# Performance work log

Hardware: AMD Instinct MI355X
Metric: run time of the kernel (lower is better)

## Reference

```python
import jax, jax.numpy as jnp
import numpy as np

NUM_EXPERTS = 8
HIDDEN = 1024
INTER = 2048
TOKENS = 2048
TOP_K = 2


def setup_inputs() -> dict:
    key = jax.random.key(0)
    k1, k2, k3, k4, k5 = jax.random.split(key, 5)
    hidden_states = jax.random.normal(k1, (TOKENS, HIDDEN), dtype=jnp.float32)
    top_k_index = jax.random.randint(k2, (TOKENS, TOP_K), 0, NUM_EXPERTS, dtype=jnp.int64)
    top_k_weights = jax.random.uniform(k3, (TOKENS, TOP_K), dtype=jnp.float32)
    # parameters, scaled like typical init
    gate_up_proj = jax.random.normal(k4, (NUM_EXPERTS, 2 * INTER, HIDDEN), dtype=jnp.float32) * (HIDDEN ** -0.5)
    down_proj = jax.random.normal(k5, (NUM_EXPERTS, HIDDEN, INTER), dtype=jnp.float32) * (INTER ** -0.5)
    return {
        "hidden_states": hidden_states,
        "top_k_index": top_k_index,
        "top_k_weights": top_k_weights,
        "gate_up_proj": gate_up_proj,
        "down_proj": down_proj,
    }


def reference(hidden_states, top_k_index, top_k_weights, gate_up_proj, down_proj):
    # combine weights per (token, expert): w[t, e] = sum_k 1[idx[t,k]==e] * tw[t,k]
    one_hot = jax.nn.one_hot(top_k_index, NUM_EXPERTS, dtype=hidden_states.dtype)  # [T, K, E]
    combine = jnp.einsum("tke,tk->te", one_hot, top_k_weights)  # [T, E]

    out = jnp.zeros_like(hidden_states)
    # fixed small loop over experts (structural, not a data dim)
    for e in range(NUM_EXPERTS):
        gu = hidden_states @ gate_up_proj[e].T  # [T, 2I]
        gate, up = jnp.split(gu, 2, axis=-1)
        h = jax.nn.gelu(gate, approximate=True) * up  # gelu_pytorch_tanh
        y = h @ down_proj[e].T  # [T, H]
        out = out + y * combine[:, e][:, None]
    return out
```

## Files before the change

kernel.cpp:

```cpp
#include <hip/hip_runtime.h>
#include <stdint.h>

#define T_TOK  2048
#define HID    1024
#define INTERN 2048
#define NEXP   8
#define MAXPOS 5248

typedef __attribute__((ext_vector_type(8))) short          bf16x8;
typedef __attribute__((ext_vector_type(4))) float          f32x4;
typedef __attribute__((ext_vector_type(8))) unsigned short u16x8;
typedef __attribute__((ext_vector_type(4))) unsigned short u16x4;

__device__ __forceinline__ unsigned short f32_to_bf16(float f) {
  unsigned int u = __float_as_uint(f);
  unsigned int r = (u + 0x7FFFu + ((u >> 16) & 1u)) >> 16;
  return (unsigned short)r;
}

__device__ __forceinline__ float bf16_to_f32(unsigned short h) {
  unsigned int u = ((unsigned int)h) << 16;
  return __uint_as_float(u);
}

__device__ __forceinline__ void gload_lds16(const void* g, void* l) {
  __builtin_amdgcn_global_load_lds(
      (const __attribute__((address_space(1))) unsigned int*)g,
      (__attribute__((address_space(3))) unsigned int*)l, 16, 0, 0);
}

__device__ __forceinline__ u16x8 cvt8(float4 a, float4 b) {
  union { u16x8 s; unsigned int u[4]; } r;
  asm("v_cvt_pk_bf16_f32 %0, %1, %2" : "=v"(r.u[0]) : "v"(a.x), "v"(a.y));
  asm("v_cvt_pk_bf16_f32 %0, %1, %2" : "=v"(r.u[1]) : "v"(a.z), "v"(a.w));
  asm("v_cvt_pk_bf16_f32 %0, %1, %2" : "=v"(r.u[2]) : "v"(b.x), "v"(b.y));
  asm("v_cvt_pk_bf16_f32 %0, %1, %2" : "=v"(r.u[3]) : "v"(b.z), "v"(b.w));
  return r.s;
}

__device__ __forceinline__ bf16x8 cvt8b(float4 a, float4 b) {
  union { u16x8 s; bf16x8 b; } r2;
  r2.s = cvt8(a, b);
  return r2.b;
}

#define WAIT_VM0()    asm volatile("s_waitcnt vmcnt(0)" ::: "memory")
#define WAIT_VM4()    asm volatile("s_waitcnt vmcnt(4)" ::: "memory")
#define WAIT_LGKM0()  asm volatile("s_waitcnt lgkmcnt(0)" ::: "memory")
#define SCHED_FENCE() __builtin_amdgcn_sched_barrier(0)

__global__ void route_kernel(const int* __restrict__ tki,
                             const float* __restrict__ tkw,
                             int* __restrict__ counts,
                             int* __restrict__ offsets,
                             int* __restrict__ tok_list,
                             float* __restrict__ w_list,
                             int* __restrict__ pos_map,
                             float* __restrict__ wgt_map) {
  __shared__ int scnt[NEXP];
  __shared__ int soff[NEXP];
  int tid = threadIdx.x;
  if (tid < NEXP) scnt[tid] = 0;
  __syncthreads();
  for (int t = tid; t < T_TOK; t += 256) {
    int e0 = tki[2 * t] & 7;
    int e1 = tki[2 * t + 1] & 7;
    float w0 = tkw[2 * t];
    float w1 = tkw[2 * t + 1];
    if (e0 == e1) {
      int p = atomicAdd(&scnt[e0], 1);
      tok_list[e0 * T_TOK + p] = t;
      w_list [e0 * T_TOK + p] = w0 + w1;
      pos_map[2 * t]     = (p << 3) | e0;
      wgt_map[2 * t]     = w0 + w1;
      pos_map[2 * t + 1] = -1;
      wgt_map[2 * t + 1] = 0.0f;
    } else {
      int p = atomicAdd(&scnt[e0], 1);
      tok_list[e0 * T_TOK + p] = t;
      w_list [e0 * T_TOK + p] = w0;
      pos_map[2 * t]     = (p << 3) | e0;
      wgt_map[2 * t]     = w0;
      int q = atomicAdd(&scnt[e1], 1);
      tok_list[e1 * T_TOK + q] = t;
      w_list [e1 * T_TOK + q] = w1;
      pos_map[2 * t + 1] = (q << 3) | e1;
      wgt_map[2 * t + 1] = w1;
    }
  }
  __syncthreads();
  if (tid == 0) {
    int acc = 0;
    for (int e = 0; e < NEXP; ++e) {
      counts[e]  = scnt[e];
      offsets[e] = acc;
      soff[e]    = acc;
      acc += ((scnt[e] + 127) >> 7) << 7;
    }
  }
  __syncthreads();
  for (int i = tid; i < 2 * T_TOK; i += 256) {
    int v = pos_map[i];
    if (v >= 0) pos_map[i] = soff[v & 7] + (v >> 3);
  }
}

__global__ void gather_cvt_x_kernel(const float* __restrict__ hidden,
                                    const int* __restrict__ counts,
                                    const int* __restrict__ offsets,
                                    const int* __restrict__ tok_list,
                                    unsigned short* __restrict__ xg) {
  int p = blockIdx.x * 2 + (threadIdx.x >> 7);
  int c = threadIdx.x & 127;
  int e = 0;
#pragma unroll
  for (int k = 1; k < NEXP; ++k) if (p >= offsets[k]) e = k;
  int r = p - offsets[e];
  float4 a = {0.f, 0.f, 0.f, 0.f}, b = {0.f, 0.f, 0.f, 0.f};
  if (r < counts[e]) {
    int tok = tok_list[e * T_TOK + r];
    const float4* src = (const float4*)(hidden + (size_t)tok * HID + c * 8);
    a = src[0]; b = src[1];
  }
  *((u16x8*)(xg + (size_t)(p >> 7) * 131072 + c * 1024 + (p & 127) * 8)) = cvt8(a, b);
}

__global__ __launch_bounds__(256, 4)
void gemm1_kernel(const unsigned short* __restrict__ xg,
                  const float* __restrict__ gup,
                  const int* __restrict__ counts,
                  const int* __restrict__ offsets,
                  unsigned short* __restrict__ hbuf) {
  int e  = blockIdx.z;
  int Ne = counts[e];
  int m0 = blockIdx.y * 128;
  if (m0 >= Ne) return;
  int n0  = blockIdx.x * 64;
  int off = offsets[e];

  __shared__ __align__(16) float Gf[2][2][4][64][4];
  __shared__ __align__(16) float Uf[2][2][4][64][4];

  int tid  = threadIdx.x;
  int lane = tid & 63;
  int wave = tid >> 6;
  int wm = wave >> 1;
  int wn = wave & 1;
  int kg4 = lane >> 4;
  int rl  = lane & 15;

  const unsigned short* afbase = xg + (size_t)((off + m0) >> 7) * (HID * 128)
                               + rl * 8 + wm * 512;

  int brow = tid & 63;
  int bfq  = tid >> 6;
  const float* gsrcD = gup + (size_t)e * (2 * INTERN) * HID + (size_t)(n0 + brow) * HID + bfq * 4;
  const float* usrcD = gsrcD + (size_t)INTERN * HID;

  f32x4 accg[4][2], accu[4][2];
#pragma unroll
  for (int m = 0; m < 4; ++m)
#pragma unroll
    for (int n = 0; n < 2; ++n) {
      accg[m][n] = (f32x4){0.f, 0.f, 0.f, 0.f};
      accu[m][n] = (f32x4){0.f, 0.f, 0.f, 0.f};
    }

  const int NT = HID / 32;

  bf16x8 af0, af1, af2, af3;

  {
    char* gb = (char*)&Gf[0][0][0][0][0];
    char* ub = (char*)&Uf[0][0][0][0][0];
    gload_lds16(gsrcD,      gb + (size_t)tid * 16);
    gload_lds16(gsrcD + 16, gb + 4096 + (size_t)tid * 16);
    gload_lds16(usrcD,      ub + (size_t)tid * 16);
    gload_lds16(usrcD + 16, ub + 4096 + (size_t)tid * 16);
    const unsigned short* ap = afbase + (size_t)kg4 * 1024;
    af0 = *((const bf16x8*)(ap));
    af1 = *((const bf16x8*)(ap + 128));
    af2 = *((const bf16x8*)(ap + 256));
    af3 = *((const bf16x8*)(ap + 384));
    WAIT_VM0(); SCHED_FENCE();
    __builtin_amdgcn_s_barrier(); SCHED_FENCE();
  }

  int cur = 0;
  for (int t = 0; t < NT; ++t) {
    int nxt = cur ^ 1;
    {
      int kb = (t + 1 < NT) ? (t + 1) * 32 : 0;
      char* gb = (char*)&Gf[nxt][0][0][0][0];
      char* ub = (char*)&Uf[nxt][0][0][0][0];
      gload_lds16(gsrcD + kb,      gb + (size_t)tid * 16);
      gload_lds16(gsrcD + kb + 16, gb + 4096 + (size_t)tid * 16);
      gload_lds16(usrcD + kb,      ub + (size_t)tid * 16);
      gload_lds16(usrcD + kb + 16, ub + 4096 + (size_t)tid * 16);
    }
    SCHED_FENCE();
    {
      int half = kg4 >> 1;
      int fq0  = (kg4 & 1) * 2;
      bf16x8 gf[2], uf[2];
#pragma unroll
      for (int n = 0; n < 2; ++n) {
        int r_ = wn * 32 + n * 16 + rl;
        float4 ga = *((const float4*)&Gf[cur][half][fq0][r_][0]);
        float4 gb2 = *((const float4*)&Gf[cur][half][fq0 + 1][r_][0]);
        float4 ua = *((const float4*)&Uf[cur][half][fq0][r_][0]);
        float4 ub2 = *((const float4*)&Uf[cur][half][fq0 + 1][r_][0]);
        gf[n] = cvt8b(ga, gb2);
        uf[n] = cvt8b(ua, ub2);
      }
      int tn = (t + 1 < NT) ? t + 1 : 0;
      const unsigned short* apn = afbase + (size_t)(tn * 4 + kg4) * 1024;
#pragma unroll
      for (int n = 0; n < 2; ++n) {
        accg[0][n] = __builtin_amdgcn_mfma_f32_16x16x32_bf16(af0, gf[n], accg[0][n], 0, 0, 0);
        accu[0][n] = __builtin_amdgcn_mfma_f32_16x16x32_bf16(af0, uf[n], accu[0][n], 0, 0, 0);
      }
      af0 = *((const bf16x8*)(apn));
#pragma unroll
      for (int n = 0; n < 2; ++n) {
        accg[1][n] = __builtin_amdgcn_mfma_f32_16x16x32_bf16(af1, gf[n], accg[1][n], 0, 0, 0);
        accu[1][n] = __builtin_amdgcn_mfma_f32_16x16x32_bf16(af1, uf[n], accu[1][n], 0, 0, 0);
      }
      af1 = *((const bf16x8*)(apn + 128));
#pragma unroll
      for (int n = 0; n < 2; ++n) {
        accg[2][n] = __builtin_amdgcn_mfma_f32_16x16x32_bf16(af2, gf[n], accg[2][n], 0, 0, 0);
        accu[2][n] = __builtin_amdgcn_mfma_f32_16x16x32_bf16(af2, uf[n], accu[2][n], 0, 0, 0);
      }
      af2 = *((const bf16x8*)(apn + 256));
#pragma unroll
      for (int n = 0; n < 2; ++n) {
        accg[3][n] = __builtin_amdgcn_mfma_f32_16x16x32_bf16(af3, gf[n], accg[3][n], 0, 0, 0);
        accu[3][n] = __builtin_amdgcn_mfma_f32_16x16x32_bf16(af3, uf[n], accu[3][n], 0, 0, 0);
      }
      af3 = *((const bf16x8*)(apn + 384));
    }
    WAIT_VM0(); SCHED_FENCE();
    __builtin_amdgcn_s_barrier(); SCHED_FENCE();
    cur = nxt;
  }

  int rq = lane >> 4;
  size_t hb_base = (size_t)((off + m0) >> 7) * (INTERN * 128);
#pragma unroll
  for (int m = 0; m < 4; ++m) {
#pragma unroll
    for (int n = 0; n < 2; ++n) {
      int col = n0 + wn * 32 + n * 16 + rl;
      size_t cbase = hb_base + (size_t)(col >> 3) * 1024 + (col & 7);
#pragma unroll
      for (int j = 0; j < 4; ++j) {
        int lr = wm * 64 + m * 16 + rq * 4 + j;
        if (m0 + lr < Ne) {
          float gv = accg[m][n][j];
          float uv = accu[m][n][j];
          float tt2 = gv + 0.044715f * gv * gv * gv;
          float a  = gv / (1.0f + __expf(-1.5957691216f * tt2));
          hbuf[cbase + (size_t)lr * 8] = f32_to_bf16(a * uv);
        }
      }
    }
  }
}

__global__ __launch_bounds__(256, 2)
void gemm2_kernel(const unsigned short* __restrict__ hbuf,
                  const float* __restrict__ down,
                  const int* __restrict__ counts,
                  const int* __restrict__ offsets,
                  unsigned short* __restrict__ ybuf) {
  int e  = blockIdx.z;
  int Ne = counts[e];
  int m0 = blockIdx.y * 128;
  if (m0 >= Ne) return;
  int n0  = blockIdx.x * 64;
  int off = offsets[e];

  __shared__ __align__(16) unsigned short As[2][8][128][8];
  __shared__ __align__(16) unsigned short Bs[2][8][64][8];

  int tid  = threadIdx.x;
  int lane = tid & 63;
  int wave = tid >> 6;
  int wm = wave >> 1;
  int wn = wave & 1;

  const unsigned short* asrc = hbuf + (size_t)((off + m0) >> 7) * (INTERN * 128);

  int brow = tid >> 2;
  int bq   = tid & 3;
  int kgw0 = bq * 2, kgw1 = bq * 2 + 1;
  const float* bsrc = down + (size_t)e * HID * INTERN + (size_t)(n0 + brow) * INTERN + bq * 16;

  f32x4 acc[4][2];
#pragma unroll
  for (int m = 0; m < 4; ++m)
#pragma unroll
    for (int n = 0; n < 2; ++n) acc[m][n] = (f32x4){0.f, 0.f, 0.f, 0.f};

  float4 b0, b1, b2, b3;

  {
    char* base = (char*)&As[0][0][0][0];
#pragma unroll
    for (int o = 0; o < 4; ++o)
      gload_lds16(asrc + o * 2048 + (size_t)tid * 8, base + o * 4096 + (size_t)tid * 16);
    const float4* bp = (const float4*)bsrc;
    float4 t0 = bp[0], t1 = bp[1], t2 = bp[2], t3 = bp[3];
    *((u16x8*)&Bs[0][kgw0][brow ^ kgw0][0]) = cvt8(t0, t1);
    *((u16x8*)&Bs[0][kgw1][brow ^ kgw1][0]) = cvt8(t2, t3);
    const float4* bp1 = (const float4*)(bsrc + 64);
    b0 = bp1[0]; b1 = bp1[1]; b2 = bp1[2]; b3 = bp1[3];
    WAIT_LGKM0(); SCHED_FENCE();
  }

  int cur = 0;
  const int NT = INTERN / 64;
  for (int t = 0; t < NT; ++t) {
    WAIT_VM4(); SCHED_FENCE();
    __builtin_amdgcn_s_barrier(); SCHED_FENCE();
    int nxt = cur ^ 1;
    int ka = (t + 1 < NT) ? (t + 1) * 64 : 0;
    {
      char* base = (char*)&As[nxt][0][0][0];
      const unsigned short* ak = asrc + (size_t)ka * 128;
#pragma unroll
      for (int o = 0; o < 4; ++o)
        gload_lds16(ak + o * 2048 + (size_t)tid * 8, base + o * 4096 + (size_t)tid * 16);
    }
    SCHED_FENCE();
#pragma unroll
    for (int kk = 0; kk < 2; ++kk) {
      int kg = kk * 4 + (lane >> 4);
      int rl = lane & 15;
      bf16x8 af[4], bfv[2];
#pragma unroll
      for (int m = 0; m < 4; ++m)
        af[m] = *((const bf16x8*)&As[cur][kg][wm * 64 + m * 16 + rl][0]);
#pragma unroll
      for (int n = 0; n < 2; ++n)
        bfv[n] = *((const bf16x8*)&Bs[cur][kg][(wn * 32 + n * 16 + rl) ^ kg][0]);
#pragma unroll
      for (int m = 0; m < 4; ++m)
#pragma unroll
        for (int n = 0; n < 2; ++n)
          acc[m][n] = __builtin_amdgcn_mfma_f32_16x16x32_bf16(af[m], bfv[n], acc[m][n], 0, 0, 0);
    }
    *((u16x8*)&Bs[nxt][kgw0][brow ^ kgw0][0]) = cvt8(b0, b1);
    *((u16x8*)&Bs[nxt][kgw1][brow ^ kgw1][0]) = cvt8(b2, b3);
    SCHED_FENCE();
    {
      int kb = (t + 2 < NT) ? (t + 2) * 64 : 0;
      const float4* bp = (const float4*)(bsrc + kb);
      b0 = bp[0]; b1 = bp[1]; b2 = bp[2]; b3 = bp[3];
    }
    WAIT_LGKM0(); SCHED_FENCE();
    cur = nxt;
  }
  WAIT_VM0();

  int rl = lane & 15;
  int rq = lane >> 4;
#pragma unroll
  for (int m = 0; m < 4; ++m) {
#pragma unroll
    for (int n = 0; n < 2; ++n) {
      int col = n0 + wn * 32 + n * 16 + rl;
#pragma unroll
      for (int j = 0; j < 4; ++j) {
        int lr = wm * 64 + m * 16 + rq * 4 + j;
        if (m0 + lr < Ne)
          ybuf[(size_t)(off + m0 + lr) * HID + col] = f32_to_bf16(acc[m][n][j]);
      }
    }
  }
}

__global__ void combine_kernel(const int* __restrict__ pos_map,
                               const float* __restrict__ wgt_map,
                               const unsigned short* __restrict__ ybuf,
                               float* __restrict__ out) {
  int i  = blockIdx.x * 256 + threadIdx.x;
  int t  = i >> 7;
  int c8 = i & 127;
  int p0 = pos_map[2 * t];
  int p1 = pos_map[2 * t + 1];
  float w0 = wgt_map[2 * t];
  float w1 = wgt_map[2 * t + 1];
  float acc[8];
#pragma unroll
  for (int j = 0; j < 8; ++j) acc[j] = 0.f;
  if (p0 >= 0) {
    u16x8 v = *((const u16x8*)(ybuf + (size_t)p0 * HID + c8 * 8));
#pragma unroll
    for (int j = 0; j < 8; ++j) acc[j] += w0 * bf16_to_f32(v[j]);
  }
  if (p1 >= 0) {
    u16x8 v = *((const u16x8*)(ybuf + (size_t)p1 * HID + c8 * 8));
#pragma unroll
    for (int j = 0; j < 8; ++j) acc[j] += w1 * bf16_to_f32(v[j]);
  }
  float4 o0 = make_float4(acc[0], acc[1], acc[2], acc[3]);
  float4 o1 = make_float4(acc[4], acc[5], acc[6], acc[7]);
  float4* dst = (float4*)(out + (size_t)t * HID + c8 * 8);
  dst[0] = o0;
  dst[1] = o1;
}

extern "C" void kernel_launch(void* const* d_in, const int* in_sizes, int n_in,
                              void* d_out, int out_size, void* d_ws, size_t ws_size,
                              hipStream_t stream) {
  (void)in_sizes; (void)n_in; (void)out_size;
  const float* hidden = (const float*)d_in[0];
  const int*   tki    = (const int*)d_in[1];
  const float* tkw    = (const float*)d_in[2];
  const float* gup    = (const float*)d_in[3];
  const float* down   = (const float*)d_in[4];
  float* out = (float*)d_out;
  char*  ws  = (char*)d_ws;

  int*   counts   = (int*)  (ws + 0);
  int*   offsets  = (int*)  (ws + 64);
  int*   tok_list = (int*)  (ws + 256);
  int*   pos_map  = (int*)  (ws + 65792);
  float* wgt_map  = (float*)(ws + 82176);
  float* w_list   = (float*)(ws + 98560);
  unsigned short* hbuf = (unsigned short*)(ws + 4358400);
  unsigned short* ybuf = (unsigned short*)(ws + 25854208);
  unsigned short* xg   = ybuf;

  if (ws_size < 36602112ull) return;

  hipLaunchKernelGGL(route_kernel, dim3(1), dim3(256), 0, stream,
                     tki, tkw, counts, offsets, tok_list, w_list, pos_map, wgt_map);
  hipLaunchKernelGGL(gather_cvt_x_kernel, dim3(MAXPOS / 2), dim3(256), 0, stream,
                     hidden, counts, offsets, tok_list, xg);
  hipLaunchKernelGGL(gemm1_kernel, dim3(INTERN / 64, T_TOK / 128, NEXP), dim3(256), 0, stream,
                     xg, gup, counts, offsets, hbuf);
  hipLaunchKernelGGL(gemm2_kernel, dim3(HID / 64, T_TOK / 128, NEXP), dim3(256), 0, stream,
                     hbuf, down, counts, offsets, ybuf);
  hipLaunchKernelGGL(combine_kernel, dim3(T_TOK * HID / 8 / 256), dim3(256), 0, stream,
                     pos_map, wgt_map, ybuf, out);
}
```

Baseline: 173.4 us.

## Triple-buffer gemm1 loads and stage activation tiles through LDS

The gate/up GEMM now keeps a three-stage LDS ring buffer, prefetching two K-tiles ahead and waiting with vmcnt(6) rather than draining all loads each iteration. The bf16 activation tile, which each wave used to load directly from global memory into registers, is now DMA'd into LDS alongside the weights and read from there. This aims to hide global memory latency. In exchange it roughly triples LDS use per block and drops the launch-bounds occupancy hint from 4 to 2.

```diff
diff --git a/kernel.cpp b/kernel.cpp
--- a/kernel.cpp
+++ b/kernel.cpp
@@ -46,6 +46,7 @@
 
 #define WAIT_VM0()    asm volatile("s_waitcnt vmcnt(0)" ::: "memory")
 #define WAIT_VM4()    asm volatile("s_waitcnt vmcnt(4)" ::: "memory")
+#define WAIT_VM6()    asm volatile("s_waitcnt vmcnt(6)" ::: "memory")
 #define WAIT_LGKM0()  asm volatile("s_waitcnt lgkmcnt(0)" ::: "memory")
 #define SCHED_FENCE() __builtin_amdgcn_sched_barrier(0)
 
@@ -125,7 +126,7 @@
   *((u16x8*)(xg + (size_t)(p >> 7) * 131072 + c * 1024 + (p & 127) * 8)) = cvt8(a, b);
 }
 
-__global__ __launch_bounds__(256, 4)
+__global__ __launch_bounds__(256, 2)
 void gemm1_kernel(const unsigned short* __restrict__ xg,
                   const float* __restrict__ gup,
                   const int* __restrict__ counts,
@@ -138,8 +139,9 @@
   int n0  = blockIdx.x * 64;
   int off = offsets[e];
 
-  __shared__ __align__(16) float Gf[2][2][4][64][4];
-  __shared__ __align__(16) float Uf[2][2][4][64][4];
+  __shared__ __align__(16) unsigned short As[3][4][128][8];
+  __shared__ __align__(16) float          Gf[3][2][4][64][4];
+  __shared__ __align__(16) float          Uf[3][2][4][64][4];
 
   int tid  = threadIdx.x;
   int lane = tid & 63;
@@ -149,8 +151,7 @@
   int kg4 = lane >> 4;
   int rl  = lane & 15;
 
-  const unsigned short* afbase = xg + (size_t)((off + m0) >> 7) * (HID * 128)
-                               + rl * 8 + wm * 512;
+  const unsigned short* abase = xg + (size_t)((off + m0) >> 7) * (HID * 128);
 
   int brow = tid & 63;
   int bfq  = tid >> 6;
@@ -168,82 +169,60 @@
 
   const int NT = HID / 32;
 
-  bf16x8 af0, af1, af2, af3;
-
-  {
-    char* gb = (char*)&Gf[0][0][0][0][0];
-    char* ub = (char*)&Uf[0][0][0][0][0];
-    gload_lds16(gsrcD,      gb + (size_t)tid * 16);
-    gload_lds16(gsrcD + 16, gb + 4096 + (size_t)tid * 16);
-    gload_lds16(usrcD,      ub + (size_t)tid * 16);
-    gload_lds16(usrcD + 16, ub + 4096 + (size_t)tid * 16);
-    const unsigned short* ap = afbase + (size_t)kg4 * 1024;
-    af0 = *((const bf16x8*)(ap));
-    af1 = *((const bf16x8*)(ap + 128));
-    af2 = *((const bf16x8*)(ap + 256));
-    af3 = *((const bf16x8*)(ap + 384));
-    WAIT_VM0(); SCHED_FENCE();
-    __builtin_amdgcn_s_barrier(); SCHED_FENCE();
-  }
-
-  int cur = 0;
+#define G1DMA(BUF, T)                                                                     \
+  {                                                                                       \
+    int tt_ = ((T) < NT) ? (T) : 0;                                                       \
+    const unsigned short* a_ = abase + (size_t)tt_ * 4096;                                \
+    gload_lds16(a_ + (size_t)tid * 8,        (char*)&As[BUF][0][0][0] + (size_t)tid * 16);\
+    gload_lds16(a_ + 2048 + (size_t)tid * 8, (char*)&As[BUF][0][0][0] + 4096 + (size_t)tid * 16);\
+    const float* g_ = gsrcD + tt_ * 32;                                                   \
+    const float* u_ = usrcD + tt_ * 32;                                                   \
+    gload_lds16(g_,      (char*)&Gf[BUF][0][0][0][0] + (size_t)tid * 16);                 \
+    gload_lds16(g_ + 16, (char*)&Gf[BUF][0][0][0][0] + 4096 + (size_t)tid * 16);          \
+    gload_lds16(u_,      (char*)&Uf[BUF][0][0][0][0] + (size_t)tid * 16);                 \
+    gload_lds16(u_ + 16, (char*)&Uf[BUF][0][0][0][0] + 4096 + (size_t)tid * 16);          \
+  }
+
+  G1DMA(0, 0);
+  G1DMA(1, 1);
+  WAIT_VM6(); SCHED_FENCE();
+  __builtin_amdgcn_s_barrier(); SCHED_FENCE();
+
   for (int t = 0; t < NT; ++t) {
-    int nxt = cur ^ 1;
-    {
-      int kb = (t + 1 < NT) ? (t + 1) * 32 : 0;
-      char* gb = (char*)&Gf[nxt][0][0][0][0];
-      char* ub = (char*)&Uf[nxt][0][0][0][0];
-      gload_lds16(gsrcD + kb,      gb + (size_t)tid * 16);
-      gload_lds16(gsrcD + kb + 16, gb + 4096 + (size_t)tid * 16);
-      gload_lds16(usrcD + kb,      ub + (size_t)tid * 16);
-      gload_lds16(usrcD + kb + 16, ub + 4096 + (size_t)tid * 16);
-    }
+    int cb = t % 3;
+    int pb = (t + 2) % 3;
+    G1DMA(pb, t + 2);
     SCHED_FENCE();
     {
       int half = kg4 >> 1;
       int fq0  = (kg4 & 1) * 2;
-      bf16x8 gf[2], uf[2];
+      bf16x8 af[4], gf[2], uf[2];
+#pragma unroll
+      for (int m = 0; m < 4; ++m)
+        af[m] = *((const bf16x8*)&As[cb][kg4][wm * 64 + m * 16 + rl][0]);
 #pragma unroll
       for (int n = 0; n < 2; ++n) {
         int r_ = wn * 32 + n * 16 + rl;
-        float4 ga = *((const float4*)&Gf[cur][half][fq0][r_][0]);
-        float4 gb2 = *((const float4*)&Gf[cur][half][fq0 + 1][r_][0]);
-        float4 ua = *((const float4*)&Uf[cur][half][fq0][r_][0]);
-        float4 ub2 = *((const float4*)&Uf[cur][half][fq0 + 1][r_][0]);
+        float4 ga  = *((const float4*)&Gf[cb][half][fq0][r_][0]);
+        float4 gb2 = *((const float4*)&Gf[cb][half][fq0 + 1][r_][0]);
+        float4 ua  = *((const float4*)&Uf[cb][half][fq0][r_][0]);
+        float4 ub2 = *((const float4*)&Uf[cb][half][fq0 + 1][r_][0]);
         gf[n] = cvt8b(ga, gb2);
         uf[n] = cvt8b(ua, ub2);
       }
-      int tn = (t + 1 < NT) ? t + 1 : 0;
-      const unsigned short* apn = afbase + (size_t)(tn * 4 + kg4) * 1024;
-#pragma unroll
-      for (int n = 0; n < 2; ++n) {
-        accg[0][n] = __builtin_amdgcn_mfma_f32_16x16x32_bf16(af0, gf[n], accg[0][n], 0, 0, 0);
-        accu[0][n] = __builtin_amdgcn_mfma_f32_16x16x32_bf16(af0, uf[n], accu[0][n], 0, 0, 0);
-      }
-      af0 = *((const bf16x8*)(apn));
-#pragma unroll
-      for (int n = 0; n < 2; ++n) {
-        accg[1][n] = __builtin_amdgcn_mfma_f32_16x16x32_bf16(af1, gf[n], accg[1][n], 0, 0, 0);
-        accu[1][n] = __builtin_amdgcn_mfma_f32_16x16x32_bf16(af1, uf[n], accu[1][n], 0, 0, 0);
-      }
-      af1 = *((const bf16x8*)(apn + 128));
-#pragma unroll
-      for (int n = 0; n < 2; ++n) {
-        accg[2][n] = __builtin_amdgcn_mfma_f32_16x16x32_bf16(af2, gf[n], accg[2][n], 0, 0, 0);
-        accu[2][n] = __builtin_amdgcn_mfma_f32_16x16x32_bf16(af2, uf[n], accu[2][n], 0, 0, 0);
-      }
-      af2 = *((const bf16x8*)(apn + 256));
-#pragma unroll
-      for (int n = 0; n < 2; ++n) {
-        accg[3][n] = __builtin_amdgcn_mfma_f32_16x16x32_bf16(af3, gf[n], accg[3][n], 0, 0, 0);
-        accu[3][n] = __builtin_amdgcn_mfma_f32_16x16x32_bf16(af3, uf[n], accu[3][n], 0, 0, 0);
-      }
-      af3 = *((const bf16x8*)(apn + 384));
-    }
-    WAIT_VM0(); SCHED_FENCE();
+#pragma unroll
+      for (int m = 0; m < 4; ++m)
+#pragma unroll
+        for (int n = 0; n < 2; ++n) {
+          accg[m][n] = __builtin_amdgcn_mfma_f32_16x16x32_bf16(af[m], gf[n], accg[m][n], 0, 0, 0);
+          accu[m][n] = __builtin_amdgcn_mfma_f32_16x16x32_bf16(af[m], uf[n], accu[m][n], 0, 0, 0);
+        }
+    }
+    WAIT_VM6(); SCHED_FENCE();
     __builtin_amdgcn_s_barrier(); SCHED_FENCE();
-    cur = nxt;
-  }
+  }
+  WAIT_VM0();
+#undef G1DMA
 
   int rq = lane >> 4;
   size_t hb_base = (size_t)((off + m0) >> 7) * (INTERN * 128);
```

New measurement: 184.5 us. 6.4% more time.
